# Kernel optimization log

Measured on AMD Instinct MI355X. Metric: run time of the kernel, lower is better.

The kernel has to match this reference:

```python
import jax, jax.numpy as jnp
import numpy as np

D_STATE = 64
D_CONV = 5
HEADDIM = 64
EXPAND = 2


def setup_inputs() -> dict:
    key = jax.random.key(0)
    ks = jax.random.split(key, 12)
    b, ch, h, w = 4, 128, 64, 64
    d_inner = EXPAND * ch
    nheads = d_inner // HEADDIM
    conv_ch = d_inner + 2 * D_STATE
    d_in_proj = 2 * d_inner + 2 * D_STATE + nheads
    s = lambda k, shape, scale: jax.random.normal(k, shape, jnp.float32) * scale
    return {
        "noisy": s(ks[0], (b, ch, h, w), 1.0),
        "aux": s(ks[1], (b, ch, h, w), 1.0),
        "ln_gamma": jnp.ones((ch,), jnp.float32),
        "ln_beta": jnp.zeros((ch,), jnp.float32),
        "in_proj_w": s(ks[2], (d_in_proj, ch), ch ** -0.5),
        "conv_w": s(ks[3], (conv_ch, D_CONV), D_CONV ** -0.5),
        "conv_b": s(ks[4], (conv_ch,), 0.02),
        "A_log": jnp.log(jnp.linspace(1.0, 16.0, nheads)).astype(jnp.float32),
        "dt_bias": s(ks[5], (nheads,), 0.1),
        "D": jnp.ones((nheads,), jnp.float32),
        "rms_w": jnp.ones((d_inner,), jnp.float32),
        "out_proj_w": s(ks[6], (ch, d_inner), d_inner ** -0.5),
        "ff_w1": s(ks[7], (ch, ch, 3, 3), (ch * 9) ** -0.5),
        "ff_b1": jnp.zeros((ch,), jnp.float32),
        "ff_w2": s(ks[8], (ch, ch, 3, 3), (ch * 9) ** -0.5),
        "ff_b2": jnp.zeros((ch,), jnp.float32),
    }


def _mamba2(u, in_proj_w, conv_w, conv_b, A_log, dt_bias, D_skip, rms_w, out_proj_w):
    # u: (b, L, d_model). Mamba2 with ngroups=1, headdim=64.
    b, L, d = u.shape
    d_inner = EXPAND * d
    nheads = d_inner // HEADDIM
    zxbcdt = u @ in_proj_w.T  # (b, L, 2*d_inner + 2*d_state + nheads)
    z = zxbcdt[..., :d_inner]
    xBC = zxbcdt[..., d_inner:2 * d_inner + 2 * D_STATE]
    dt = jax.nn.softplus(zxbcdt[..., -nheads:] + dt_bias)  # (b, L, h)
    # causal depthwise conv1d along L + SiLU
    xBC_c = jnp.transpose(xBC, (0, 2, 1))  # (b, C, L)
    xBC_c = jax.lax.conv_general_dilated(
        xBC_c, conv_w[:, None, :], (1,), [(D_CONV - 1, 0)],
        feature_group_count=xBC_c.shape[1])
    xBC = jax.nn.silu(jnp.transpose(xBC_c + conv_b[None, :, None], (0, 2, 1)))
    x = xBC[..., :d_inner]
    B = xBC[..., d_inner:d_inner + D_STATE]  # (b, L, n)
    C = xBC[..., d_inner + D_STATE:]         # (b, L, n)
    A = -jnp.exp(A_log)                      # (h,)
    xh = x.reshape(b, L, nheads, HEADDIM)    # (b, L, h, p)
    dA = jnp.exp(dt * A)                     # (b, L, h)

    def step(hstate, inputs):
        dA_t, dt_t, x_t, B_t, C_t = inputs
        hstate = hstate * dA_t[:, :, None, None] + jnp.einsum('bh,bhp,bn->bhpn', dt_t, x_t, B_t)
        y_t = jnp.einsum('bhpn,bn->bhp', hstate, C_t)
        return hstate, y_t

    init = jnp.zeros((b, nheads, HEADDIM, D_STATE), u.dtype)
    xs = (jnp.moveaxis(dA, 1, 0), jnp.moveaxis(dt, 1, 0), jnp.moveaxis(xh, 1, 0),
          jnp.moveaxis(B, 1, 0), jnp.moveaxis(C, 1, 0))
    _, ys = jax.lax.scan(step, init, xs)
    y = jnp.moveaxis(ys, 0, 1) + xh * D_skip[None, None, :, None]  # (b, L, h, p)
    y = y.reshape(b, L, d_inner)
    # gated RMSNorm: rmsnorm(y * silu(z)) * weight
    y = y * jax.nn.silu(z)
    y = y * jax.lax.rsqrt(jnp.mean(y * y, axis=-1, keepdims=True) + 1e-5) * rms_w
    return y @ out_proj_w.T


def _conv3x3_reflect(x, w, b):
    x = jnp.pad(x, ((0, 0), (0, 0), (1, 1), (1, 1)), mode='reflect')
    return jax.lax.conv_general_dilated(x, w, (1, 1), 'VALID') + b[None, :, None, None]


def reference(noisy, aux, ln_gamma, ln_beta, in_proj_w, conv_w, conv_b, A_log,
              dt_bias, D, rms_w, out_proj_w, ff_w1, ff_b1, ff_w2, ff_b2):
    b, c, h, w = noisy.shape
    flat = jnp.transpose(noisy, (0, 2, 3, 1)).reshape(b, h * w, c)
    mu = jnp.mean(flat, axis=-1, keepdims=True)
    var = jnp.var(flat, axis=-1, keepdims=True)
    normed = (flat - mu) * jax.lax.rsqrt(var + 1e-5) * ln_gamma + ln_beta
    m = _mamba2(normed, in_proj_w, conv_w, conv_b, A_log, dt_bias, D, rms_w, out_proj_w)
    m = jnp.transpose(m.reshape(b, h, w, c), (0, 3, 1, 2))
    y = noisy + m
    ff = jax.nn.relu(_conv3x3_reflect(y, ff_w1, ff_b1))
    ff = jax.nn.relu(_conv3x3_reflect(ff, ff_w2, ff_b2))
    y = y + ff
    return (y, aux)
```

## Files before the change

kernel.cpp:

```cpp
#include <hip/hip_runtime.h>
#include <cstddef>

#define B_      4
#define C_      128
#define L_      4096
#define DIN     256
#define NH      4
#define HD      64
#define DS      64
#define CONVCH  384
#define DPROJ   644
#define CHUNK   64
#define NCHUNK  64

typedef short bf16x8 __attribute__((ext_vector_type(8)));
typedef float floatx16 __attribute__((ext_vector_type(16)));

__device__ __forceinline__ float siluf(float v) { return v / (1.f + __expf(-v)); }

__device__ __forceinline__ ushort f2bf(float v) {
  unsigned u = __float_as_uint(v);
  unsigned r = (u + 0x7fff + ((u >> 16) & 1)) >> 16;
  return (ushort)r;
}
__device__ __forceinline__ float bf2f(ushort h) {
  return __uint_as_float((unsigned)h << 16);
}

__global__ __launch_bounds__(256) void wprep_all(
    const float* __restrict__ ipw, ushort* __restrict__ Bh, ushort* __restrict__ Bl,
    const float* __restrict__ opw, ushort* __restrict__ Oh, ushort* __restrict__ Ol,
    const float* __restrict__ fw1, ushort* __restrict__ Wt1,
    const float* __restrict__ fw2, ushort* __restrict__ Wt2) {
  int bi = blockIdx.x;
  int t = threadIdx.x;
  if (bi < 176) {
    int e = bi * 256 + t;
    int d = e >> 6;
    int c0 = (e & 63) * 2;
    int kk = c0 >> 4;
    int l = (d & 31) + 32 * ((c0 & 15) >> 3);
    int j = c0 & 7;
    size_t off = (((size_t)(d >> 5)) * 8 + kk) * 512 + l * 8 + j;
    float v0 = d < 644 ? ipw[(size_t)d * 128 + c0] : 0.f;
    float v1 = d < 644 ? ipw[(size_t)d * 128 + c0 + 1] : 0.f;
    ushort h0 = f2bf(v0), h1 = f2bf(v1);
    *(unsigned*)(Bh + off) = (unsigned)h0 | ((unsigned)h1 << 16);
    *(unsigned*)(Bl + off) = (unsigned)f2bf(v0 - bf2f(h0)) |
                             ((unsigned)f2bf(v1 - bf2f(h1)) << 16);
  } else if (bi < 304) {
    int e = (bi - 176) * 256 + t;
    int d = e >> 8;
    int c = e & 255;
    size_t f = ((size_t)(d >> 5) * 16 + (c >> 4)) * 512 +
               ((d & 31) + 32 * ((c & 15) >> 3)) * 8 + (c & 7);
    float v = opw[(size_t)d * 256 + c];
    ushort h = f2bf(v);
    Oh[f] = h;
    Ol[f] = f2bf(v - bf2f(h));
  } else {
    const float* fw = bi < 432 ? fw1 : fw2;
    ushort* Wt = bi < 432 ? Wt1 : Wt2;
    int co = (bi - 304) & 127;
    int cb = co >> 5;
    for (int e = t; e < 1152; e += 256) {
      int tap = e >> 7;
      int ci = e & 127;
      int kk = ci >> 4, k16 = ci & 15;
      int l = (co & 31) + 32 * (k16 >> 3);
      int off = ((tap * 8 + kk) * 4 + cb) * 512 + l * 8 + (k16 & 7);
      Wt[off] = f2bf(fw[(size_t)co * 1152 + ci * 9 + tap]);
    }
  }
}

__global__ __launch_bounds__(1024) void ln_gemm1(
    const float* __restrict__ noisy, const float* __restrict__ gamma,
    const float* __restrict__ beta,
    const ushort* __restrict__ Bh, const ushort* __restrict__ Bl,
    float* __restrict__ ZX) {
  int row = blockIdx.x, b = blockIdx.y;
  int t = threadIdx.x;
  __shared__ float tile[64 * 129];
  __shared__ float ps[16][64], pq[16][64];
  __shared__ float smu[64], srs[64];
  __shared__ __align__(16) ushort AhL[8192];
  __shared__ __align__(16) ushort AlL[8192];
  int px = t & 63, cg = t >> 6;
  float s = 0.f, s2 = 0.f;
  const float* src = noisy + ((size_t)b * C_) * L_ + row * 64;
  for (int i = 0; i < 8; ++i) {
    int c = cg * 8 + i;
    float v = src[(size_t)c * L_ + px];
    tile[px * 129 + c] = v;
    s += v; s2 += v * v;
  }
  ps[cg][px] = s; pq[cg][px] = s2;
  __syncthreads();
  if (t < 64) {
    float a = 0.f, qq = 0.f;
#pragma unroll
    for (int g = 0; g < 16; ++g) { a += ps[g][t]; qq += pq[g][t]; }
    float mu = a * (1.f / 128.f);
    float var = qq * (1.f / 128.f) - mu * mu;
    smu[t] = mu;
    srs[t] = rsqrtf(var + 1e-5f);
  }
  __syncthreads();
  for (int idx = t; idx < 4096; idx += 1024) {
    int p2 = idx >> 6;
    int c0 = (idx & 63) * 2;
    float v0 = (tile[p2 * 129 + c0] - smu[p2]) * srs[p2] * gamma[c0] + beta[c0];
    float v1 = (tile[p2 * 129 + c0 + 1] - smu[p2]) * srs[p2] * gamma[c0 + 1] + beta[c0 + 1];
    int kk = c0 >> 4;
    int l = (p2 & 31) + 32 * ((c0 & 15) >> 3);
    int j = c0 & 7;
    int off = ((p2 >> 5) * 8 + kk) * 512 + l * 8 + j;
    ushort h0 = f2bf(v0), h1 = f2bf(v1);
    *(unsigned*)(AhL + off) = (unsigned)h0 | ((unsigned)h1 << 16);
    *(unsigned*)(AlL + off) = (unsigned)f2bf(v0 - bf2f(h0)) |
                              ((unsigned)f2bf(v1 - bf2f(h1)) << 16);
  }
  __syncthreads();
  int wv = t >> 6, lane = t & 63;
  int db = wv & 1, pb = (wv >> 1) & 1, bq = wv >> 2;
  int rowadd = 4 * (lane >> 5);
  for (int bn = bq; bn < 11; bn += 4) {
    floatx16 acc;
#pragma unroll
    for (int i = 0; i < 16; ++i) acc[i] = 0.f;
    size_t bbase = ((size_t)(bn * 2 + db) * 8) * 64 + lane;
    const bf16x8* pBh = (const bf16x8*)Bh + bbase;
    const bf16x8* pBl = (const bf16x8*)Bl + bbase;
#pragma unroll
    for (int kk = 0; kk < 8; ++kk) {
      bf16x8 ah = *(const bf16x8*)(AhL + (pb * 8 + kk) * 512 + lane * 8);
      bf16x8 al = *(const bf16x8*)(AlL + (pb * 8 + kk) * 512 + lane * 8);
      bf16x8 bh = pBh[kk * 64];
      bf16x8 bl = pBl[kk * 64];
      acc = __builtin_amdgcn_mfma_f32_32x32x16_bf16(ah, bh, acc, 0, 0, 0);
      acc = __builtin_amdgcn_mfma_f32_32x32x16_bf16(al, bh, acc, 0, 0, 0);
      acc = __builtin_amdgcn_mfma_f32_32x32x16_bf16(ah, bl, acc, 0, 0, 0);
    }
    int d = bn * 64 + db * 32 + (lane & 31);
    if (d < 644) {
#pragma unroll
      for (int r = 0; r < 16; ++r) {
        int rowm = (r & 3) + 8 * (r >> 2) + rowadd;
        int pix = row * 64 + pb * 32 + rowm;
        ZX[((size_t)(b * L_ + pix)) * DPROJ + d] = acc[r];
      }
    }
  }
}

__global__ __launch_bounds__(384) void conv1d_silu(
    const float* __restrict__ ZX, const float* __restrict__ cw,
    const float* __restrict__ cb, float* __restrict__ XBC) {
  int ch = threadIdx.x;
  int l0 = blockIdx.x * 16, b = blockIdx.y;
  const float* base = ZX + ((size_t)b * L_) * DPROJ + DIN + ch;
  float w0 = cw[ch * 5], w1 = cw[ch * 5 + 1], w2 = cw[ch * 5 + 2],
        w3 = cw[ch * 5 + 3], w4 = cw[ch * 5 + 4];
  float bias = cb[ch];
  float win[20];
#pragma unroll
  for (int i = 0; i < 20; ++i) {
    int ll = l0 - 4 + i;
    win[i] = ll >= 0 ? base[(size_t)ll * DPROJ] : 0.f;
  }
  float* dst = XBC + ((size_t)(b * L_ + l0)) * CONVCH + ch;
#pragma unroll
  for (int j = 0; j < 16; ++j) {
    float acc = bias + w0 * win[j] + w1 * win[j + 1] + w2 * win[j + 2] +
                w3 * win[j + 3] + w4 * win[j + 4];
    dst[(size_t)j * CONVCH] = siluf(acc);
  }
}

#define UPDA(k, B4, C4) \
  st[4*k+0] = st[4*k+0]*da + cf*B4.x; y0 += st[4*k+0]*C4.x; \
  st[4*k+1] = st[4*k+1]*da + cf*B4.y; y1 += st[4*k+1]*C4.y; \
  st[4*k+2] = st[4*k+2]*da + cf*B4.z; y2 += st[4*k+2]*C4.z; \
  st[4*k+3] = st[4*k+3]*da + cf*B4.w; y3 += st[4*k+3]*C4.w;

__global__ __launch_bounds__(256, 4) void scan_passA(
    const float* __restrict__ XBC, const float* __restrict__ ZX,
    const float* __restrict__ dt_bias, const float* __restrict__ A_log,
    float* __restrict__ YL, float* __restrict__ SC, float* __restrict__ PC,
    float* __restrict__ CUM) {
  int chunk = blockIdx.x, h = blockIdx.y, b = blockIdx.z;
  int t = threadIdx.x;
  int p = t >> 2, q = t & 3;
  int bh = b * NH + h;
  __shared__ float sdt[CHUNK], sda[CHUNK];
  __shared__ float sB[32][64];
  __shared__ float sCc[32][64];
  __shared__ float sx[32][64];
  if (t < CHUNK) {
    int l = chunk * CHUNK + t;
    float v = ZX[((size_t)(b * L_ + l)) * DPROJ + 640 + h] + dt_bias[h];
    float dt = v > 20.f ? v : log1pf(expf(v));
    sdt[t] = dt;
    sda[t] = expf(dt * -expf(A_log[h]));
  }
  size_t rowbase = ((size_t)b * L_ + (size_t)chunk * CHUNK) * CONVCH;
  float* __restrict__ yl = YL + ((size_t)b * L_ + (size_t)chunk * CHUNK) * DIN + h * HD + p;
  float* __restrict__ cumout = CUM + (size_t)bh * L_ + chunk * CHUNK;
  float st[16];
#pragma unroll
  for (int j = 0; j < 16; ++j) st[j] = 0.f;
  float cum = 1.f;
  for (int half = 0; half < 2; ++half) {
    __syncthreads();
#pragma unroll
    for (int i = 0; i < 2; ++i) {
      int e = t + i * 256;
      int row = e >> 4, c4 = (e & 15) * 4;
      const float* gsrc = XBC + rowbase + (size_t)(half * 32 + row) * CONVCH;
      *(float4*)&sB[row][c4]  = *(const float4*)(gsrc + DIN + c4);
      *(float4*)&sCc[row][c4] = *(const float4*)(gsrc + DIN + DS + c4);
      *(float4*)&sx[row][c4]  = *(const float4*)(gsrc + h * HD + c4);
    }
    __syncthreads();
#pragma unroll 4
    for (int tl = 0; tl < 32; ++tl) {
      int tg = half * 32 + tl;
      float da = sda[tg], dtv = sdt[tg];
      float x = sx[tl][p];
      float cf = dtv * x;
      const float4* br = (const float4*)&sB[tl][q * 16];
      const float4* cr = (const float4*)&sCc[tl][q * 16];
      float4 B0 = br[0], B1 = br[1], B2 = br[2], B3 = br[3];
      float4 C0 = cr[0], C1 = cr[1], C2 = cr[2], C3 = cr[3];
      float y0 = 0.f, y1 = 0.f, y2 = 0.f, y3 = 0.f;
      UPDA(0, B0, C0) UPDA(1, B1, C1) UPDA(2, B2, C2) UPDA(3, B3, C3)
      float y = (y0 + y1) + (y2 + y3);
      y += __shfl_xor(y, 1);
      y += __shfl_xor(y, 2);
      cum *= da;
      if (q == 0) yl[(size_t)tg * DIN] = y;
      if (t == 0) cumout[tg] = cum;
    }
  }
  float* scp = SC + ((size_t)bh * NCHUNK + chunk) * 4096 + p * 64 + q * 16;
  *(float4*)(scp + 0)  = make_float4(st[0], st[1], st[2], st[3]);
  *(float4*)(scp + 4)  = make_float4(st[4], st[5], st[6], st[7]);
  *(float4*)(scp + 8)  = make_float4(st[8], st[9], st[10], st[11]);
  *(float4*)(scp + 12) = make_float4(st[12], st[13], st[14], st[15]);
  if (t == 0) PC[bh * NCHUNK + chunk] = cum;
}

__global__ __launch_bounds__(256) void scan_passB(
    float* __restrict__ SC, const float* __restrict__ PC) {
  int bh = blockIdx.x >> 4;
  int eg = blockIdx.x & 15;
  int e = eg * 256 + threadIdx.x;
  float h = 0.f;
#pragma unroll 8
  for (int c = 0; c < NCHUNK; ++c) {
    size_t idx = ((size_t)bh * NCHUNK + c) * 4096 + e;
    float s = SC[idx];
    float pcv = PC[bh * NCHUNK + c];
    SC[idx] = h;
    h = h * pcv + s;
  }
}

__global__ __launch_bounds__(1024) void passC_gate(
    const float* __restrict__ XBC, const float* __restrict__ SC,
    const float* __restrict__ CUM, const float* __restrict__ Dp,
    const float* __restrict__ YL, const float* __restrict__ ZX,
    const float* __restrict__ rmsw,
    const ushort* __restrict__ Oh, const ushort* __restrict__ Ol,
    const float* __restrict__ noisy, float* __restrict__ YRES) {
  __shared__ float yt[16384];
  __shared__ __align__(16) ushort fr[32768];
  int chunk = blockIdx.x, b = blockIdx.y;
  int t = threadIdx.x;
  int h = t >> 8, t1 = t & 255;
  int p = t1 >> 2, q = t1 & 3;
  int bh = b * NH + h;
  size_t pix0g = (size_t)b * L_ + (size_t)chunk * CHUNK;

  const float* hi = SC + ((size_t)bh * NCHUNK + chunk) * 4096 + p * 64 + q * 16;
  float hreg[16];
  {
    float4 v;
    v = *(const float4*)(hi + 0);  hreg[0] = v.x; hreg[1] = v.y; hreg[2] = v.z; hreg[3] = v.w;
    v = *(const float4*)(hi + 4);  hreg[4] = v.x; hreg[5] = v.y; hreg[6] = v.z; hreg[7] = v.w;
    v = *(const float4*)(hi + 8);  hreg[8] = v.x; hreg[9] = v.y; hreg[10] = v.z; hreg[11] = v.w;
    v = *(const float4*)(hi + 12); hreg[12] = v.x; hreg[13] = v.y; hreg[14] = v.z; hreg[15] = v.w;
  }
  for (int i = t; i < 4096; i += 1024) {
    *(float4*)&yt[i * 4] = *(const float4*)&YL[pix0g * DIN + (size_t)i * 4];
  }
  float Dv = Dp[h];
  float* sCcf  = (float*)fr;
  float* sxf   = (float*)fr + 1024;
  float* scumf = (float*)fr + 5120;

  for (int tq = 0; tq < 4; ++tq) {
    int t0 = tq * 16;
    __syncthreads();
    {
      int row = t1 >> 4, c4 = (t1 & 15) * 4;
      const float* gsrc = XBC + (pix0g + t0 + row) * CONVCH;
      *(float4*)&sxf[h * 1024 + row * 64 + c4] = *(const float4*)(gsrc + h * HD + c4);
      if (t < 256) {
        *(float4*)&sCcf[row * 64 + c4] = *(const float4*)(gsrc + DIN + DS + c4);
      }
      if (t < 64) {
        int hh = t >> 4, i = t & 15;
        scumf[hh * 16 + i] = CUM[((size_t)(b * NH + hh)) * L_ + chunk * CHUNK + t0 + i];
      }
    }
    __syncthreads();
#pragma unroll 4
    for (int tl = 0; tl < 16; ++tl) {
      const float4* cr = (const float4*)&sCcf[tl * 64 + q * 16];
      float4 C0 = cr[0], C1 = cr[1], C2 = cr[2], C3 = cr[3];
      float x = sxf[h * 1024 + tl * 64 + p];
      float cum = scumf[h * 16 + tl];
      float y0 = 0.f, y1 = 0.f, y2 = 0.f, y3 = 0.f;
      y0 += hreg[0]*C0.x;  y1 += hreg[1]*C0.y;  y2 += hreg[2]*C0.z;  y3 += hreg[3]*C0.w;
      y0 += hreg[4]*C1.x;  y1 += hreg[5]*C1.y;  y2 += hreg[6]*C1.z;  y3 += hreg[7]*C1.w;
      y0 += hreg[8]*C2.x;  y1 += hreg[9]*C2.y;  y2 += hreg[10]*C2.z; y3 += hreg[11]*C2.w;
      y0 += hreg[12]*C3.x; y1 += hreg[13]*C3.y; y2 += hreg[14]*C3.z; y3 += hreg[15]*C3.w;
      float y = (y0 + y1) + (y2 + y3);
      y += __shfl_xor(y, 1);
      y += __shfl_xor(y, 2);
      if (q == 0) {
        yt[(t0 + tl) * 256 + h * 64 + p] += cum * y + x * Dv;
      }
    }
  }
  __syncthreads();

  ushort* AhL = fr;
  ushort* AlL = fr + 16384;
  int lp = t & 31;
  int slot = t >> 5;
  float4 w0 = *(const float4*)(rmsw + lp * 4);
  float4 w1 = *(const float4*)(rmsw + 128 + lp * 4);
  for (int it = 0; it < 2; ++it) {
    int pl = it * 32 + slot;
    const float* y = &yt[pl * 256];
    const float* z = ZX + (pix0g + pl) * DPROJ;
    float4 y0 = *(const float4*)(y + lp * 4);
    float4 y1 = *(const float4*)(y + 128 + lp * 4);
    float4 z0 = *(const float4*)(z + lp * 4);
    float4 z1 = *(const float4*)(z + 128 + lp * 4);
    float g[8];
    g[0] = y0.x * siluf(z0.x); g[1] = y0.y * siluf(z0.y);
    g[2] = y0.z * siluf(z0.z); g[3] = y0.w * siluf(z0.w);
    g[4] = y1.x * siluf(z1.x); g[5] = y1.y * siluf(z1.y);
    g[6] = y1.z * siluf(z1.z); g[7] = y1.w * siluf(z1.w);
    float ss = 0.f;
#pragma unroll
    for (int j = 0; j < 8; ++j) ss += g[j] * g[j];
    ss += __shfl_xor(ss, 16);
    ss += __shfl_xor(ss, 8);
    ss += __shfl_xor(ss, 4);
    ss += __shfl_xor(ss, 2);
    ss += __shfl_xor(ss, 1);
    float rs = rsqrtf(ss * (1.f / 256.f) + 1e-5f);
    float o[8];
    o[0] = g[0] * rs * w0.x; o[1] = g[1] * rs * w0.y;
    o[2] = g[2] * rs * w0.z; o[3] = g[3] * rs * w0.w;
    o[4] = g[4] * rs * w1.x; o[5] = g[5] * rs * w1.y;
    o[6] = g[6] * rs * w1.z; o[7] = g[7] * rs * w1.w;
#pragma unroll
    for (int grp = 0; grp < 2; ++grp) {
      int d = grp * 128 + lp * 4;
      int off = ((pl >> 5) * 16 + (d >> 4)) * 512 +
                ((pl & 31) + 32 * ((d & 15) >> 3)) * 8 + (d & 7);
      ushort h0 = f2bf(o[grp*4+0]), h1 = f2bf(o[grp*4+1]);
      ushort h2 = f2bf(o[grp*4+2]), h3 = f2bf(o[grp*4+3]);
      uint2 hv, lv;
      hv.x = (unsigned)h0 | ((unsigned)h1 << 16);
      hv.y = (unsigned)h2 | ((unsigned)h3 << 16);
      lv.x = (unsigned)f2bf(o[grp*4+0] - bf2f(h0)) | ((unsigned)f2bf(o[grp*4+1] - bf2f(h1)) << 16);
      lv.y = (unsigned)f2bf(o[grp*4+2] - bf2f(h2)) | ((unsigned)f2bf(o[grp*4+3] - bf2f(h3)) << 16);
      *(uint2*)(AhL + off) = hv;
      *(uint2*)(AlL + off) = lv;
    }
  }
  __syncthreads();

  floatx16 acc;
#pragma unroll
  for (int i = 0; i < 16; ++i) acc[i] = 0.f;
  int wv = t >> 6, lane = t & 63;
  int pb = wv >> 2, bn = (wv >> 1) & 1, db = wv & 1;
  int rowadd = 4 * (lane >> 5);
  if (wv < 8) {
    const bf16x8* pBh = (const bf16x8*)Oh;
    const bf16x8* pBl = (const bf16x8*)Ol;
    size_t bbase = ((size_t)(bn * 2 + db) * 16) * 64 + lane;
#pragma unroll
    for (int kk = 0; kk < 16; ++kk) {
      bf16x8 ah = *(const bf16x8*)(AhL + (pb * 16 + kk) * 512 + lane * 8);
      bf16x8 al = *(const bf16x8*)(AlL + (pb * 16 + kk) * 512 + lane * 8);
      bf16x8 bh = pBh[bbase + (size_t)kk * 64];
      bf16x8 bl = pBl[bbase + (size_t)kk * 64];
      acc = __builtin_amdgcn_mfma_f32_32x32x16_bf16(ah, bh, acc, 0, 0, 0);
      acc = __builtin_amdgcn_mfma_f32_32x32x16_bf16(al, bh, acc, 0, 0, 0);
      acc = __builtin_amdgcn_mfma_f32_32x32x16_bf16(ah, bl, acc, 0, 0, 0);
    }
  }
  __syncthreads();

  float* tile = (float*)fr;
  if (wv < 8) {
#pragma unroll
    for (int r = 0; r < 16; ++r) {
      int rowm = (r & 3) + 8 * (r >> 2) + rowadd;
      int rowp = pb * 32 + rowm;
      int col = bn * 64 + db * 32 + (lane & 31);
      tile[rowp * 129 + col] = acc[r];
    }
  }
  __syncthreads();
  int l0 = chunk * CHUNK;
  for (int idx = t; idx < 8192; idx += 1024) {
    int c = idx >> 6, px = idx & 63;
    size_t o = ((size_t)(b * C_ + c)) * L_ + l0 + px;
    YRES[o] = noisy[o] + tile[px * 129 + c];
  }
}

template <int MODE>
__global__ __launch_bounds__(512) void conv3x3_direct(
    const void* __restrict__ inv, const ushort* __restrict__ Wt,
    const float* __restrict__ bias, const float* __restrict__ res,
    void* __restrict__ outv) {
  __shared__ __align__(16) ushort lds[3 * 64 * 128];
  int y = blockIdx.x, b = blockIdx.y;
  int t = threadIdx.x;
  int lane = t & 63;
  int wv = t >> 6;
  int ry[3];
  ry[0] = y == 0 ? 1 : y - 1;
  ry[1] = y;
  ry[2] = y == 63 ? 62 : y + 1;
  {
    int x = lane;
    for (int u = wv; u < 48; u += 8) {
      int r = u / 16;
      int cib = u % 16;
      int ci0 = cib * 8;
      ushort vals[8];
#pragma unroll
      for (int j = 0; j < 8; ++j) {
        size_t src = ((size_t)(b * C_ + ci0 + j)) * L_ + ry[r] * 64 + x;
        if (MODE == 0) vals[j] = f2bf(((const float*)inv)[src]);
        else           vals[j] = ((const ushort*)inv)[src];
      }
      int idx = (r * 64 + x) * 128 + (cib ^ (x & 15)) * 8;
      *(int4*)&lds[idx] = *(int4*)vals;
    }
  }
  __syncthreads();
  int cb = wv >> 1, nb = wv & 1;
  int n = lane & 31, hi = lane >> 5;
  floatx16 acc0, acc1;
#pragma unroll
  for (int i = 0; i < 16; ++i) { acc0[i] = 0.f; acc1[i] = 0.f; }
  const bf16x8* pW = (const bf16x8*)Wt;
  for (int tap = 0; tap < 9; ++tap) {
    int ky = tap / 3, kx = tap % 3;
    int xg = nb * 32 + n + kx - 1;
    int xx = xg < 0 ? 1 : (xg > 63 ? 62 : xg);
    int base = (ky * 64 + xx) * 128;
    int xs = xx & 15;
#pragma unroll
    for (int kk = 0; kk < 8; ++kk) {
      bf16x8 av = pW[(size_t)((tap * 8 + kk) * 4 + cb) * 64 + lane];
      bf16x8 bv = *(const bf16x8*)&lds[base + ((kk * 2 + hi) ^ xs) * 8];
      if (kk & 1) acc1 = __builtin_amdgcn_mfma_f32_32x32x16_bf16(av, bv, acc1, 0, 0, 0);
      else        acc0 = __builtin_amdgcn_mfma_f32_32x32x16_bf16(av, bv, acc0, 0, 0, 0);
    }
  }
  int x0 = nb * 32 + (lane & 31);
  int rowadd = 4 * (lane >> 5);
#pragma unroll
  for (int r = 0; r < 16; ++r) {
    int rowm = (r & 3) + 8 * (r >> 2) + rowadd;
    int co = cb * 32 + rowm;
    size_t o = ((size_t)(b * C_ + co)) * L_ + y * 64 + x0;
    float v = fmaxf(acc0[r] + acc1[r] + bias[co], 0.f);
    if (MODE == 0) {
      ((ushort*)outv)[o] = f2bf(v);
    } else {
      ((float*)outv)[o] = v + res[o];
    }
  }
}

extern "C" void kernel_launch(void* const* d_in, const int* in_sizes, int n_in,
                              void* d_out, int out_size, void* d_ws, size_t ws_size,
                              hipStream_t stream) {
  const float* noisy   = (const float*)d_in[0];
  const float* aux     = (const float*)d_in[1];
  const float* ln_g    = (const float*)d_in[2];
  const float* ln_b    = (const float*)d_in[3];
  const float* ipw     = (const float*)d_in[4];
  const float* cw      = (const float*)d_in[5];
  const float* cbv     = (const float*)d_in[6];
  const float* A_log   = (const float*)d_in[7];
  const float* dt_bias = (const float*)d_in[8];
  const float* Dp      = (const float*)d_in[9];
  const float* rmsw    = (const float*)d_in[10];
  const float* opw     = (const float*)d_in[11];
  const float* fw1     = (const float*)d_in[12];
  const float* fb1     = (const float*)d_in[13];
  const float* fw2     = (const float*)d_in[14];
  const float* fb2     = (const float*)d_in[15];
  float* out = (float*)d_out;
  float* ws  = (float*)d_ws;

  const size_t OFF_ZX   = 0;
  const size_t OFF_XBC  = OFF_ZX + 16384UL * 644;
  const size_t OFF_SCN  = OFF_XBC + 16384UL * 384;
  const size_t OFF_WT   = OFF_SCN + 4194304UL;
  const size_t OFF_WO   = OFF_WT + 73728UL;
  const size_t OFF_CUM  = OFF_WT + 131072UL;
  const size_t OFF_YL   = OFF_CUM + 65536UL;
  const size_t OFF_PC   = OFF_YL + 16384UL * 256;
  const size_t OFF_WT2  = OFF_PC + 1024UL;
  const size_t OFF_YRES = OFF_WT2 + 73728UL;

  float* ZX   = ws + OFF_ZX;
  float* XBC  = ws + OFF_XBC;
  float* SC   = ws + OFF_SCN;
  float* CUM  = ws + OFF_CUM;
  float* YL   = ws + OFF_YL;
  float* PC   = ws + OFF_PC;
  ushort* Bnh  = (ushort*)(ws + OFF_YL);
  ushort* Bnl  = Bnh + 45056UL * 2;
  ushort* Wt1 = (ushort*)(ws + OFF_WT);
  ushort* Woh  = (ushort*)(ws + OFF_WO);
  ushort* Wol  = Woh + 32768UL;
  ushort* Wt2 = (ushort*)(ws + OFF_WT2);
  ushort* FF1 = (ushort*)(ws + OFF_SCN);
  float* YRES = ws + OFF_YRES;

  wprep_all<<<560, 256, 0, stream>>>(ipw, Bnh, Bnl, opw, Woh, Wol, fw1, Wt1, fw2, Wt2);
  ln_gemm1<<<dim3(64, 4), 1024, 0, stream>>>(noisy, ln_g, ln_b, Bnh, Bnl, ZX);
  conv1d_silu<<<dim3(L_ / 16, B_), 384, 0, stream>>>(ZX, cw, cbv, XBC);
  scan_passA<<<dim3(NCHUNK, NH, B_), 256, 0, stream>>>(XBC, ZX, dt_bias, A_log, YL, SC, PC, CUM);
  scan_passB<<<256, 256, 0, stream>>>(SC, PC);
  passC_gate<<<dim3(NCHUNK, B_), 1024, 0, stream>>>(XBC, SC, CUM, Dp, YL, ZX,
                                                    rmsw, Woh, Wol, noisy, YRES);
  conv3x3_direct<0><<<dim3(64, 4), 512, 0, stream>>>(YRES, Wt1, fb1, nullptr, FF1);
  conv3x3_direct<1><<<dim3(64, 4), 512, 0, stream>>>(FF1, Wt2, fb2, YRES, out);
  hipMemcpyAsync(out + 2097152, aux, 2097152UL * sizeof(float),
                 hipMemcpyDeviceToDevice, stream);
}
```

Measured before the change: 261.2 us.

## Compute inter-chunk state contribution in passC with split-bf16 MFMA

Replaces the per-thread FP32 dot-product loop over the chunk state (C·h) in passC_gate with a 3-pass split-bf16 MFMA GEMM, staging C in a swizzled LDS layout. The D-skip term is now applied in a separate vectorized pass. The Z gate values are prefetched into registers early, and the idle waves prefetch the noisy residual into LDS while the out-projection MFMA runs. This aims to cut the FP32 ALU and shuffle cost and hide global load latency, at the cost of extra bf16 split conversions and more register pressure.

New measurement: 244.3 us. 6.5% less time.

```diff
diff --git a/kernel.cpp b/kernel.cpp
--- a/kernel.cpp
+++ b/kernel.cpp
@@ -25,6 +25,16 @@
 }
 __device__ __forceinline__ float bf2f(ushort h) {
   return __uint_as_float((unsigned)h << 16);
+}
+
+__device__ __forceinline__ void split8(float4 v0, float4 v1, bf16x8& hi, bf16x8& lo) {
+  float f[8] = {v0.x, v0.y, v0.z, v0.w, v1.x, v1.y, v1.z, v1.w};
+#pragma unroll
+  for (int j = 0; j < 8; ++j) {
+    ushort h = f2bf(f[j]);
+    hi[j] = (short)h;
+    lo[j] = (short)f2bf(f[j] - bf2f(h));
+  }
 }
 
 __global__ __launch_bounds__(256) void wprep_all(
@@ -278,112 +288,133 @@
   __shared__ __align__(16) ushort fr[32768];
   int chunk = blockIdx.x, b = blockIdx.y;
   int t = threadIdx.x;
-  int h = t >> 8, t1 = t & 255;
-  int p = t1 >> 2, q = t1 & 3;
-  int bh = b * NH + h;
+  int wv = t >> 6, lane = t & 63;
   size_t pix0g = (size_t)b * L_ + (size_t)chunk * CHUNK;
-
-  const float* hi = SC + ((size_t)bh * NCHUNK + chunk) * 4096 + p * 64 + q * 16;
-  float hreg[16];
+  float* sCcf  = (float*)fr;
+  float* scumf = sCcf + 4096;
+
+  float4 zr[4];
   {
-    float4 v;
-    v = *(const float4*)(hi + 0);  hreg[0] = v.x; hreg[1] = v.y; hreg[2] = v.z; hreg[3] = v.w;
-    v = *(const float4*)(hi + 4);  hreg[4] = v.x; hreg[5] = v.y; hreg[6] = v.z; hreg[7] = v.w;
-    v = *(const float4*)(hi + 8);  hreg[8] = v.x; hreg[9] = v.y; hreg[10] = v.z; hreg[11] = v.w;
-    v = *(const float4*)(hi + 12); hreg[12] = v.x; hreg[13] = v.y; hreg[14] = v.z; hreg[15] = v.w;
+    int lp = t & 31, slot2 = t >> 5;
+#pragma unroll
+    for (int it = 0; it < 2; ++it) {
+      const float* z = ZX + (pix0g + it * 32 + slot2) * DPROJ;
+      zr[it * 2]     = *(const float4*)(z + lp * 4);
+      zr[it * 2 + 1] = *(const float4*)(z + 128 + lp * 4);
+    }
   }
   for (int i = t; i < 4096; i += 1024) {
     *(float4*)&yt[i * 4] = *(const float4*)&YL[pix0g * DIN + (size_t)i * 4];
   }
-  float Dv = Dp[h];
-  float* sCcf  = (float*)fr;
-  float* sxf   = (float*)fr + 1024;
-  float* scumf = (float*)fr + 5120;
-
-  for (int tq = 0; tq < 4; ++tq) {
-    int t0 = tq * 16;
-    __syncthreads();
-    {
-      int row = t1 >> 4, c4 = (t1 & 15) * 4;
-      const float* gsrc = XBC + (pix0g + t0 + row) * CONVCH;
-      *(float4*)&sxf[h * 1024 + row * 64 + c4] = *(const float4*)(gsrc + h * HD + c4);
-      if (t < 256) {
-        *(float4*)&sCcf[row * 64 + c4] = *(const float4*)(gsrc + DIN + DS + c4);
-      }
-      if (t < 64) {
-        int hh = t >> 4, i = t & 15;
-        scumf[hh * 16 + i] = CUM[((size_t)(b * NH + hh)) * L_ + chunk * CHUNK + t0 + i];
-      }
-    }
-    __syncthreads();
-#pragma unroll 4
-    for (int tl = 0; tl < 16; ++tl) {
-      const float4* cr = (const float4*)&sCcf[tl * 64 + q * 16];
-      float4 C0 = cr[0], C1 = cr[1], C2 = cr[2], C3 = cr[3];
-      float x = sxf[h * 1024 + tl * 64 + p];
-      float cum = scumf[h * 16 + tl];
-      float y0 = 0.f, y1 = 0.f, y2 = 0.f, y3 = 0.f;
-      y0 += hreg[0]*C0.x;  y1 += hreg[1]*C0.y;  y2 += hreg[2]*C0.z;  y3 += hreg[3]*C0.w;
-      y0 += hreg[4]*C1.x;  y1 += hreg[5]*C1.y;  y2 += hreg[6]*C1.z;  y3 += hreg[7]*C1.w;
-      y0 += hreg[8]*C2.x;  y1 += hreg[9]*C2.y;  y2 += hreg[10]*C2.z; y3 += hreg[11]*C2.w;
-      y0 += hreg[12]*C3.x; y1 += hreg[13]*C3.y; y2 += hreg[14]*C3.z; y3 += hreg[15]*C3.w;
-      float y = (y0 + y1) + (y2 + y3);
-      y += __shfl_xor(y, 1);
-      y += __shfl_xor(y, 2);
-      if (q == 0) {
-        yt[(t0 + tl) * 256 + h * 64 + p] += cum * y + x * Dv;
-      }
+  {
+    int px = t >> 4, slot = t & 15;
+    float4 cv = *(const float4*)(XBC + (pix0g + px) * CONVCH + DIN + DS + slot * 4);
+    ((float4*)sCcf)[px * 16 + (slot ^ (px & 7))] = cv;
+    if (t < 256) {
+      int hh = t >> 6, px2 = t & 63;
+      scumf[t] = CUM[((size_t)(b * NH + hh)) * L_ + chunk * CHUNK + px2];
+    }
+  }
+  __syncthreads();
+
+  {
+    int px = t >> 4, c4 = (t & 15) * 4;
+    const float* xs = XBC + (pix0g + px) * CONVCH;
+#pragma unroll
+    for (int hh = 0; hh < 4; ++hh) {
+      float4 xv = *(const float4*)(xs + hh * HD + c4);
+      float dv = Dp[hh];
+      float* dst = &yt[px * 256 + hh * 64 + c4];
+      dst[0] += xv.x * dv; dst[1] += xv.y * dv;
+      dst[2] += xv.z * dv; dst[3] += xv.w * dv;
+    }
+  }
+  __syncthreads();
+
+  {
+    int h1 = wv >> 2, ptile = (wv >> 1) & 1, pxtile = wv & 1;
+    int arow = pxtile * 32 + (lane & 31);
+    const float* Sb = SC + (((size_t)(b * NH + h1)) * NCHUNK + chunk) * 4096 +
+                      (size_t)(ptile * 32 + (lane & 31)) * 64 + (lane >> 5) * 8;
+    const float4* av = (const float4*)sCcf + arow * 16;
+    int s0 = (lane >> 5) * 2;
+    floatx16 acc;
+#pragma unroll
+    for (int i = 0; i < 16; ++i) acc[i] = 0.f;
+#pragma unroll
+    for (int kk = 0; kk < 4; ++kk) {
+      float4 b0 = *(const float4*)(Sb + kk * 16);
+      float4 b1 = *(const float4*)(Sb + kk * 16 + 4);
+      int sa = kk * 4 + s0;
+      float4 a0 = av[sa ^ (arow & 7)];
+      float4 a1 = av[(sa + 1) ^ (arow & 7)];
+      bf16x8 ah, al, bh, bl;
+      split8(a0, a1, ah, al);
+      split8(b0, b1, bh, bl);
+      acc = __builtin_amdgcn_mfma_f32_32x32x16_bf16(ah, bh, acc, 0, 0, 0);
+      acc = __builtin_amdgcn_mfma_f32_32x32x16_bf16(al, bh, acc, 0, 0, 0);
+      acc = __builtin_amdgcn_mfma_f32_32x32x16_bf16(ah, bl, acc, 0, 0, 0);
+    }
+    int col = h1 * 64 + ptile * 32 + (lane & 31);
+    int radd = 4 * (lane >> 5);
+#pragma unroll
+    for (int r = 0; r < 16; ++r) {
+      int pxl = (r & 3) + 8 * (r >> 2) + radd;
+      int px = pxtile * 32 + pxl;
+      yt[px * 256 + col] += acc[r] * scumf[h1 * 64 + px];
     }
   }
   __syncthreads();
 
   ushort* AhL = fr;
   ushort* AlL = fr + 16384;
-  int lp = t & 31;
-  int slot = t >> 5;
-  float4 w0 = *(const float4*)(rmsw + lp * 4);
-  float4 w1 = *(const float4*)(rmsw + 128 + lp * 4);
-  for (int it = 0; it < 2; ++it) {
-    int pl = it * 32 + slot;
-    const float* y = &yt[pl * 256];
-    const float* z = ZX + (pix0g + pl) * DPROJ;
-    float4 y0 = *(const float4*)(y + lp * 4);
-    float4 y1 = *(const float4*)(y + 128 + lp * 4);
-    float4 z0 = *(const float4*)(z + lp * 4);
-    float4 z1 = *(const float4*)(z + 128 + lp * 4);
-    float g[8];
-    g[0] = y0.x * siluf(z0.x); g[1] = y0.y * siluf(z0.y);
-    g[2] = y0.z * siluf(z0.z); g[3] = y0.w * siluf(z0.w);
-    g[4] = y1.x * siluf(z1.x); g[5] = y1.y * siluf(z1.y);
-    g[6] = y1.z * siluf(z1.z); g[7] = y1.w * siluf(z1.w);
-    float ss = 0.f;
-#pragma unroll
-    for (int j = 0; j < 8; ++j) ss += g[j] * g[j];
-    ss += __shfl_xor(ss, 16);
-    ss += __shfl_xor(ss, 8);
-    ss += __shfl_xor(ss, 4);
-    ss += __shfl_xor(ss, 2);
-    ss += __shfl_xor(ss, 1);
-    float rs = rsqrtf(ss * (1.f / 256.f) + 1e-5f);
-    float o[8];
-    o[0] = g[0] * rs * w0.x; o[1] = g[1] * rs * w0.y;
-    o[2] = g[2] * rs * w0.z; o[3] = g[3] * rs * w0.w;
-    o[4] = g[4] * rs * w1.x; o[5] = g[5] * rs * w1.y;
-    o[6] = g[6] * rs * w1.z; o[7] = g[7] * rs * w1.w;
-#pragma unroll
-    for (int grp = 0; grp < 2; ++grp) {
-      int d = grp * 128 + lp * 4;
-      int off = ((pl >> 5) * 16 + (d >> 4)) * 512 +
-                ((pl & 31) + 32 * ((d & 15) >> 3)) * 8 + (d & 7);
-      ushort h0 = f2bf(o[grp*4+0]), h1 = f2bf(o[grp*4+1]);
-      ushort h2 = f2bf(o[grp*4+2]), h3 = f2bf(o[grp*4+3]);
-      uint2 hv, lv;
-      hv.x = (unsigned)h0 | ((unsigned)h1 << 16);
-      hv.y = (unsigned)h2 | ((unsigned)h3 << 16);
-      lv.x = (unsigned)f2bf(o[grp*4+0] - bf2f(h0)) | ((unsigned)f2bf(o[grp*4+1] - bf2f(h1)) << 16);
-      lv.y = (unsigned)f2bf(o[grp*4+2] - bf2f(h2)) | ((unsigned)f2bf(o[grp*4+3] - bf2f(h3)) << 16);
-      *(uint2*)(AhL + off) = hv;
-      *(uint2*)(AlL + off) = lv;
+  {
+    int lp = t & 31;
+    int slot = t >> 5;
+    float4 w0 = *(const float4*)(rmsw + lp * 4);
+    float4 w1 = *(const float4*)(rmsw + 128 + lp * 4);
+#pragma unroll
+    for (int it = 0; it < 2; ++it) {
+      int pl = it * 32 + slot;
+      const float* y = &yt[pl * 256];
+      float4 y0 = *(const float4*)(y + lp * 4);
+      float4 y1 = *(const float4*)(y + 128 + lp * 4);
+      float4 z0 = zr[it * 2];
+      float4 z1 = zr[it * 2 + 1];
+      float g[8];
+      g[0] = y0.x * siluf(z0.x); g[1] = y0.y * siluf(z0.y);
+      g[2] = y0.z * siluf(z0.z); g[3] = y0.w * siluf(z0.w);
+      g[4] = y1.x * siluf(z1.x); g[5] = y1.y * siluf(z1.y);
+      g[6] = y1.z * siluf(z1.z); g[7] = y1.w * siluf(z1.w);
+      float ss = 0.f;
+#pragma unroll
+      for (int j = 0; j < 8; ++j) ss += g[j] * g[j];
+      ss += __shfl_xor(ss, 16);
+      ss += __shfl_xor(ss, 8);
+      ss += __shfl_xor(ss, 4);
+      ss += __shfl_xor(ss, 2);
+      ss += __shfl_xor(ss, 1);
+      float rs = rsqrtf(ss * (1.f / 256.f) + 1e-5f);
+      float o[8];
+      o[0] = g[0] * rs * w0.x; o[1] = g[1] * rs * w0.y;
+      o[2] = g[2] * rs * w0.z; o[3] = g[3] * rs * w0.w;
+      o[4] = g[4] * rs * w1.x; o[5] = g[5] * rs * w1.y;
+      o[6] = g[6] * rs * w1.z; o[7] = g[7] * rs * w1.w;
+#pragma unroll
+      for (int grp = 0; grp < 2; ++grp) {
+        int d = grp * 128 + lp * 4;
+        int off = ((pl >> 5) * 16 + (d >> 4)) * 512 +
+                  ((pl & 31) + 32 * ((d & 15) >> 3)) * 8 + (d & 7);
+        ushort h0 = f2bf(o[grp*4+0]), h1 = f2bf(o[grp*4+1]);
+        ushort h2 = f2bf(o[grp*4+2]), h3 = f2bf(o[grp*4+3]);
+        uint2 hv, lv;
+        hv.x = (unsigned)h0 | ((unsigned)h1 << 16);
+        hv.y = (unsigned)h2 | ((unsigned)h3 << 16);
+        lv.x = (unsigned)f2bf(o[grp*4+0] - bf2f(h0)) | ((unsigned)f2bf(o[grp*4+1] - bf2f(h1)) << 16);
+        lv.y = (unsigned)f2bf(o[grp*4+2] - bf2f(h2)) | ((unsigned)f2bf(o[grp*4+3] - bf2f(h3)) << 16);
+        *(uint2*)(AhL + off) = hv;
+        *(uint2*)(AlL + off) = lv;
+      }
     }
   }
   __syncthreads();
@@ -391,7 +422,6 @@
   floatx16 acc;
 #pragma unroll
   for (int i = 0; i < 16; ++i) acc[i] = 0.f;
-  int wv = t >> 6, lane = t & 63;
   int pb = wv >> 2, bn = (wv >> 1) & 1, db = wv & 1;
   int rowadd = 4 * (lane >> 5);
   if (wv < 8) {
@@ -408,6 +438,14 @@
       acc = __builtin_amdgcn_mfma_f32_32x32x16_bf16(al, bh, acc, 0, 0, 0);
       acc = __builtin_amdgcn_mfma_f32_32x32x16_bf16(ah, bl, acc, 0, 0, 0);
     }
+  } else {
+    int t2 = t - 512;
+#pragma unroll
+    for (int k = 0; k < 16; ++k) {
+      int idx = t2 + k * 512;
+      int c = idx >> 6, px = idx & 63;
+      yt[idx] = noisy[((size_t)(b * C_ + c)) * L_ + chunk * CHUNK + px];
+    }
   }
   __syncthreads();
 
@@ -422,11 +460,10 @@
     }
   }
   __syncthreads();
-  int l0 = chunk * CHUNK;
   for (int idx = t; idx < 8192; idx += 1024) {
     int c = idx >> 6, px = idx & 63;
-    size_t o = ((size_t)(b * C_ + c)) * L_ + l0 + px;
-    YRES[o] = noisy[o] + tile[px * 129 + c];
+    size_t o = ((size_t)(b * C_ + c)) * L_ + chunk * CHUNK + px;
+    YRES[o] = yt[idx] + tile[px * 129 + c];
   }
 }
 
```
